# Kernel tuning notes

Hardware: AMD Instinct MI355X
Metric: run time of the kernel (lower is better)

## Reference

```python
import jax, jax.numpy as jnp
import numpy as np

B, M, D, H, C = 256, 512, 768, 8, 768


def setup_inputs() -> dict:
    key = jax.random.key(0)
    ks = jax.random.split(key, 12)
    rn = lambda k, shp, s=1.0: jax.random.normal(k, shp, dtype=jnp.float32) * s
    w = 1.0 / np.sqrt(D)
    return dict(
        controller_state=rn(ks[0], (B, C)),
        write_data=rn(ks[1], (B, D)),
        memory=rn(ks[2], (M, D), 0.1),
        in_proj_w=rn(ks[3], (3 * D, D), w), in_proj_b=jnp.zeros((3 * D,), jnp.float32),
        out_w=rn(ks[4], (D, D), w), out_b=jnp.zeros((D,), jnp.float32),
        read_w=rn(ks[5], (D, C), w), read_b=jnp.zeros((D,), jnp.float32),
        write_w=rn(ks[6], (D, C), w), write_b=jnp.zeros((D,), jnp.float32),
        erase_w=rn(ks[7], (D, C), w), erase_b=jnp.zeros((D,), jnp.float32),
        ug_w=rn(ks[8], (1, C + D), w), ug_b=jnp.zeros((1,), jnp.float32),
        fg_w=rn(ks[9], (1, C + D), w), fg_b=jnp.zeros((1,), jnp.float32),
    )


def _mha(q, kv, in_proj_w, in_proj_b, out_w, out_b, num_heads):
    # q: [B,1,D] query, kv: [B,M,D] keys=values. Matches torch.nn.MultiheadAttention
    # (batch_first, eval mode -> no dropout, average_attn_weights=True).
    b, m, d = kv.shape
    dh = d // num_heads
    wq, wk, wv = jnp.split(in_proj_w, 3, axis=0)
    bq, bk, bv = jnp.split(in_proj_b, 3, axis=0)
    qh = (q @ wq.T + bq).reshape(b, 1, num_heads, dh).transpose(0, 2, 1, 3)   # [B,H,1,dh]
    kh = (kv @ wk.T + bk).reshape(b, m, num_heads, dh).transpose(0, 2, 1, 3)  # [B,H,M,dh]
    vh = (kv @ wv.T + bv).reshape(b, m, num_heads, dh).transpose(0, 2, 1, 3)
    scores = jnp.einsum('bhqd,bhkd->bhqk', qh, kh) / jnp.sqrt(jnp.float32(dh))
    attn = jax.nn.softmax(scores, axis=-1)                                    # [B,H,1,M]
    ctx = jnp.einsum('bhqk,bhkd->bhqd', attn, vh)
    ctx = ctx.transpose(0, 2, 1, 3).reshape(b, 1, d)
    out = ctx @ out_w.T + out_b
    return out, attn.mean(axis=1)  # out [B,1,D], weights averaged over heads [B,1,M]


def reference(controller_state, write_data, memory, in_proj_w, in_proj_b,
              out_w, out_b, read_w, read_b, write_w, write_b,
              erase_w, erase_b, ug_w, ug_b, fg_w, fg_b):
    b = controller_state.shape[0]
    memory_batch = jnp.broadcast_to(memory[None], (b,) + memory.shape)        # [B,M,D]

    read_key = (controller_state @ read_w.T + read_b)[:, None, :]             # [B,1,D]
    read_data, _ = _mha(read_key, memory_batch, in_proj_w, in_proj_b, out_w, out_b, H)
    read_data = read_data[:, 0, :]                                            # [B,D]

    write_key = (controller_state @ write_w.T + write_b)[:, None, :]
    erase_vec = jax.nn.sigmoid(controller_state @ erase_w.T + erase_b)[:, None, :]  # [B,1,D]
    _, write_weights = _mha(write_key, memory_batch, in_proj_w, in_proj_b, out_w, out_b, H)
    ww = write_weights[:, 0, :]                                               # [B,M]

    combined = jnp.concatenate([controller_state, read_data], axis=-1)        # [B,C+D]
    ug = jax.nn.sigmoid(combined @ ug_w.T + ug_b)                             # [B,1]
    fg = jax.nn.sigmoid(combined @ fg_w.T + fg_b)                             # [B,1]

    erase_term = ww[:, :, None] * erase_vec * fg[:, :, None]                  # [B,M,D]
    write_term = ww[:, :, None] * write_data[:, None, :] * ug[:, :, None]     # [B,M,D]
    updated_memory = memory_batch + (write_term - erase_term)
    return read_data, updated_memory
```

## Files before the change

### kernel.cpp

```cpp
#include <hip/hip_runtime.h>
#include <hip/hip_bf16.h>
#include <math.h>

#define B_ 256
#define M_ 512
#define D_ 768
#define H_ 8
#define DH_ 96
#define C_ 768

typedef float  f32x4_t __attribute__((ext_vector_type(4)));
typedef short  s16x8   __attribute__((ext_vector_type(8)));
typedef unsigned short u16;

__device__ __forceinline__ u16 cvt_bf16(float f) {
    __hip_bfloat16 h = __float2bfloat16(f);
    union { __hip_bfloat16 h; u16 u; } v; v.h = h;
    return v.u;
}
__device__ __forceinline__ float bf16_f32(u16 h) {
    union { unsigned int u; float f; } v; v.u = ((unsigned int)h) << 16;
    return v.f;
}

#define ACC_INIT {{0,0,0,0},{0,0,0,0},{0,0,0,0},{0,0,0,0}}
#define SCALE_ 0.10206207261596577f

template<int BK>
__device__ __forceinline__ void mm64b(
    const u16* __restrict__ A, int lda, const u16* __restrict__ B, int ldb,
    int ksteps, int bRowClamp, u16* lA, u16* lB, f32x4_t* acc, int nfrag)
{
    constexpr int NL = BK / 32;
    const int t = threadIdx.x;
    const int srow = t >> 2, kq = t & 3;
    const int l = t & 63, w = t >> 6;
    const int brow = srow < bRowClamp ? srow : bRowClamp;

    s16x8 va[NL], vb[NL];
    #pragma unroll
    for (int c = 0; c < NL; ++c) {
        const int ko = (kq * NL + c) * 8;
        va[c] = *reinterpret_cast<const s16x8*>(A + (size_t)srow * lda + ko);
        vb[c] = *reinterpret_cast<const s16x8*>(B + (size_t)brow * ldb + ko);
    }

    for (int ks = 0; ks < ksteps; ++ks) {
        __syncthreads();
        #pragma unroll
        for (int c = 0; c < NL; ++c) {
            const int kb = kq * NL + c;
            *reinterpret_cast<s16x8*>(lA + (kb * 64 + srow) * 8) = va[c];
            *reinterpret_cast<s16x8*>(lB + (kb * 64 + srow) * 8) = vb[c];
        }
        __syncthreads();
        if (ks + 1 < ksteps) {
            #pragma unroll
            for (int c = 0; c < NL; ++c) {
                const int ko = (ks + 1) * BK + (kq * NL + c) * 8;
                va[c] = *reinterpret_cast<const s16x8*>(A + (size_t)srow * lda + ko);
                vb[c] = *reinterpret_cast<const s16x8*>(B + (size_t)brow * ldb + ko);
            }
        }
        #pragma unroll
        for (int ksub = 0; ksub < NL; ++ksub) {
            const int kb = (l >> 4) + ksub * 4;
            s16x8 af = *reinterpret_cast<const s16x8*>(lA + (kb * 64 + w * 16 + (l & 15)) * 8);
            #pragma unroll
            for (int nb = 0; nb < 4; ++nb) {
                if (nb < nfrag) {
                    s16x8 bf = *reinterpret_cast<const s16x8*>(lB + (kb * 64 + nb * 16 + (l & 15)) * 8);
                    acc[nb] = __builtin_amdgcn_mfma_f32_16x16x32_bf16(af, bf, acc[nb], 0, 0, 0);
                }
            }
        }
    }
}

__device__ __forceinline__ void epilogue_f32(
    const f32x4_t* acc, float* out, int ldo, int m0, int n0,
    const float* bias, int act, int nfrag)
{
    const int t = threadIdx.x, l = t & 63, w = t >> 6;
    const int mbase = m0 + w * 16 + (l >> 4) * 4;
    #pragma unroll
    for (int nb = 0; nb < 4; ++nb) {
        if (nb >= nfrag) break;
        const int col = n0 + nb * 16 + (l & 15);
        const float bv = bias ? bias[col] : 0.0f;
        #pragma unroll
        for (int r = 0; r < 4; ++r) {
            float v = acc[nb][r] + bv;
            if (act) v = 1.0f / (1.0f + expf(-v));
            out[(size_t)(mbase + r) * ldo + col] = v;
        }
    }
}

__device__ __forceinline__ void epilogue_bf16(
    const f32x4_t* acc, u16* out, int ldo, int m0, int n0,
    const float* bias, int nfrag)
{
    const int t = threadIdx.x, l = t & 63, w = t >> 6;
    const int mbase = m0 + w * 16 + (l >> 4) * 4;
    #pragma unroll
    for (int nb = 0; nb < 4; ++nb) {
        if (nb >= nfrag) break;
        const int col = n0 + nb * 16 + (l & 15);
        const float bv = bias ? bias[col] : 0.0f;
        #pragma unroll
        for (int r = 0; r < 4; ++r)
            out[(size_t)(mbase + r) * ldo + col] = cvt_bf16(acc[nb][r] + bv);
    }
}

__global__ __launch_bounds__(256) void conv_kernel(
    const float* __restrict__ mem, const float* __restrict__ cs,
    const float* __restrict__ ipw, const float* __restrict__ rw,
    const float* __restrict__ www, const float* __restrict__ ew,
    const float* __restrict__ outw, const float* __restrict__ outb,
    const float* __restrict__ ugw, const float* __restrict__ ugb,
    const float* __restrict__ fgw, const float* __restrict__ fgb,
    u16* __restrict__ memb, u16* __restrict__ csb, u16* __restrict__ ipwb,
    u16* __restrict__ rwb, u16* __restrict__ wwwb, u16* __restrict__ ewb,
    u16* __restrict__ outwb, float* __restrict__ vg, float* __restrict__ gc)
{
    __shared__ float sred[256];
    const int bid = blockIdx.x, t = threadIdx.x;

    if (bid < 2304) {
        const float* src; u16* dst; int base;
        if      (bid < 192)  { src = mem;  dst = memb;  base = bid; }
        else if (bid < 288)  { src = cs;   dst = csb;   base = bid - 192; }
        else if (bid < 1152) { src = ipw;  dst = ipwb;  base = bid - 288; }
        else if (bid < 1440) { src = rw;   dst = rwb;   base = bid - 1152; }
        else if (bid < 1728) { src = www;  dst = wwwb;  base = bid - 1440; }
        else if (bid < 2016) { src = ew;   dst = ewb;   base = bid - 1728; }
        else                 { src = outw; dst = outwb; base = bid - 2016; }
        const size_t i = ((size_t)base * 256 + t) * 8;
        float4 x = *reinterpret_cast<const float4*>(src + i);
        float4 y = *reinterpret_cast<const float4*>(src + i + 4);
        s16x8 o;
        o[0]=cvt_bf16(x.x); o[1]=cvt_bf16(x.y); o[2]=cvt_bf16(x.z); o[3]=cvt_bf16(x.w);
        o[4]=cvt_bf16(y.x); o[5]=cvt_bf16(y.y); o[6]=cvt_bf16(y.z); o[7]=cvt_bf16(y.w);
        *reinterpret_cast<s16x8*>(dst + i) = o;
    } else {
        const int lid = bid - 2304;
        const int v = lid / 12, kt = lid % 12;
        const float* gw = v == 0 ? ugw : fgw;
        const int c = t & 63, g = t >> 6;
        const int col = kt * 64 + c;
        float acc = 0.f;
        #pragma unroll 4
        for (int i = 0; i < 192; ++i) {
            const int row = g * 192 + i;
            acc += outw[(size_t)row * 768 + col] * gw[768 + row];
        }
        sred[t] = acc;
        __syncthreads();
        if (g == 0)
            vg[v * 768 + col] = sred[c] + sred[64 + c] + sred[128 + c] + sred[192 + c];
        if (kt == 0) {
            __syncthreads();
            float cp = outb[t] * gw[768 + t] + outb[t + 256] * gw[768 + t + 256]
                     + outb[t + 512] * gw[768 + t + 512];
            sred[t] = cp; __syncthreads();
            #pragma unroll
            for (int off = 128; off > 0; off >>= 1) {
                if (t < off) sred[t] += sred[t + off];
                __syncthreads();
            }
            if (t == 0) gc[v] = sred[0] + (v == 0 ? ugb[0] : fgb[0]);
        }
    }
}

__global__ __launch_bounds__(256) void stage1_kernel(
    const u16* __restrict__ memb, const u16* __restrict__ csb,
    const u16* __restrict__ ipwb, const float* __restrict__ ipb,
    const u16* __restrict__ rwb, const float* __restrict__ rb,
    const u16* __restrict__ wwwb, const float* __restrict__ ww_b,
    const u16* __restrict__ ewb, const float* __restrict__ eb,
    u16* __restrict__ khb, u16* __restrict__ vhT,
    u16* __restrict__ rwkeysb, float* __restrict__ erase)
{
    __shared__ u16 lA[8192], lB[8192];
    f32x4_t acc[4] = ACC_INIT;
    const int bid = blockIdx.x;
    if (bid < 192) {
        const int mt = bid / 24, nt = bid % 24;
        mm64b<64>(memb + (size_t)mt * 64 * 768, 768,
                  ipwb + (size_t)768 * 768 + (size_t)nt * 64 * 768, 768,
                  12, 63, lA, lB, acc, 4);
        const int t = threadIdx.x, l = t & 63, w = t >> 6;
        const int mbase = mt * 64 + w * 16 + (l >> 4) * 4;
        if (nt < 12) {
            #pragma unroll
            for (int nb = 0; nb < 4; ++nb) {
                const int col = nt * 64 + nb * 16 + (l & 15);
                const float bv = ipb[768 + col];
                #pragma unroll
                for (int r = 0; r < 4; ++r)
                    khb[(size_t)(mbase + r) * 768 + col] = cvt_bf16(acc[nb][r] + bv);
            }
        } else {
            #pragma unroll
            for (int nb = 0; nb < 4; ++nb) {
                const int cg = (nt - 12) * 64 + nb * 16 + (l & 15);
                const int h = cg / 96, d = cg % 96;
                const float bv = ipb[1536 + cg];
                u16* dst = vhT + ((size_t)h * 96 + d) * 512;
                #pragma unroll
                for (int r = 0; r < 4; ++r)
                    dst[mbase + r] = cvt_bf16(acc[nb][r] + bv);
            }
        }
    } else if (bid < 240) {
        const int lid = bid - 192, mt = lid / 12, nt = lid % 12;
        mm64b<64>(csb + (size_t)mt * 64 * 768, 768, rwb + (size_t)nt * 64 * 768, 768,
                  12, 63, lA, lB, acc, 4);
        epilogue_bf16(acc, rwkeysb, 768, mt * 64, nt * 64, rb, 4);
    } else if (bid < 288) {
        const int lid = bid - 240, mt = lid / 12, nt = lid % 12;
        mm64b<64>(csb + (size_t)mt * 64 * 768, 768, wwwb + (size_t)nt * 64 * 768, 768,
                  12, 63, lA, lB, acc, 4);
        epilogue_bf16(acc, rwkeysb + (size_t)256 * 768, 768, mt * 64, nt * 64, ww_b, 4);
    } else {
        const int lid = bid - 288, mt = lid / 12, nt = lid % 12;
        mm64b<64>(csb + (size_t)mt * 64 * 768, 768, ewb + (size_t)nt * 64 * 768, 768,
                  12, 63, lA, lB, acc, 4);
        epilogue_f32(acc, erase, 768, mt * 64, nt * 64, eb, 1, 4);
    }
}

__global__ __launch_bounds__(256) void stage2_kernel(
    const u16* __restrict__ rwkeysb, const u16* __restrict__ ipwb,
    const float* __restrict__ ipb, u16* __restrict__ qrwb)
{
    __shared__ u16 lA[8192], lB[8192];
    f32x4_t acc[4] = ACC_INIT;
    const int mt = blockIdx.x / 12, nt = blockIdx.x % 12;
    mm64b<64>(rwkeysb + (size_t)mt * 64 * 768, 768, ipwb + (size_t)nt * 64 * 768, 768,
              12, 63, lA, lB, acc, 4);
    epilogue_bf16(acc, qrwb, 768, mt * 64, nt * 64, ipb, 4);
}

__global__ __launch_bounds__(256) void scores_kernel(
    const u16* __restrict__ qrwb, const u16* __restrict__ khb, u16* __restrict__ E)
{
    __shared__ u16 lA[2048], lB[2048];
    f32x4_t acc[4] = ACC_INIT;
    const int h = blockIdx.y;
    const int mt = blockIdx.x >> 3, nt = blockIdx.x & 7;
    mm64b<32>(qrwb + (size_t)mt * 64 * 768 + h * 96, 768,
              khb + (size_t)nt * 64 * 768 + h * 96, 768, 3, 63, lA, lB, acc, 4);
    const int t = threadIdx.x, l = t & 63, w = t >> 6;
    const int mbase = mt * 64 + w * 16 + (l >> 4) * 4;
    #pragma unroll
    for (int nb = 0; nb < 4; ++nb) {
        const int col = nt * 64 + nb * 16 + (l & 15);
        #pragma unroll
        for (int r = 0; r < 4; ++r) {
            const float e = expf(fminf(acc[nb][r] * SCALE_, 30.0f));
            E[((size_t)h * 512 + mbase + r) * 512 + col] = cvt_bf16(e);
        }
    }
}

__global__ __launch_bounds__(256) void pvww_kernel(
    const u16* __restrict__ E, const u16* __restrict__ vhT, u16* __restrict__ ctxb,
    float* __restrict__ wwb)
{
    const int bid = blockIdx.x, t = threadIdx.x;
    if (bid < 64) {
        __shared__ u16 lA[8192], lB[8192];
        __shared__ float rinv[64];
        f32x4_t acc[4] = ACC_INIT;
        const int h = bid >> 3;
        const int mt = (bid >> 1) & 3, nt = bid & 1;
        const int n0 = nt * 64;
        const int nfrag = nt == 0 ? 4 : 2;
        const int bclamp = nt == 0 ? 63 : 31;

        const u16* A  = E + ((size_t)h * 512 + mt * 64) * 512;
        const u16* Bv = vhT + ((size_t)h * 96 + n0) * 512;

        const int srow = t >> 2, kq = t & 3;
        const int l = t & 63, w = t >> 6;
        const int brow = srow < bclamp ? srow : bclamp;

        s16x8 va[2], vb[2];
        #pragma unroll
        for (int c = 0; c < 2; ++c) {
            const int ko = (kq * 2 + c) * 8;
            va[c] = *reinterpret_cast<const s16x8*>(A + (size_t)srow * 512 + ko);
            vb[c] = *reinterpret_cast<const s16x8*>(Bv + (size_t)brow * 512 + ko);
        }

        float rs = 0.f;
        for (int ks = 0; ks < 8; ++ks) {
            __syncthreads();
            #pragma unroll
            for (int c = 0; c < 2; ++c) {
                const int kb = kq * 2 + c;
                *reinterpret_cast<s16x8*>(lA + (kb * 64 + srow) * 8) = va[c];
                *reinterpret_cast<s16x8*>(lB + (kb * 64 + srow) * 8) = vb[c];
            }
            #pragma unroll
            for (int c = 0; c < 2; ++c)
                #pragma unroll
                for (int j = 0; j < 8; ++j)
                    rs += bf16_f32((u16)va[c][j]);
            __syncthreads();
            if (ks + 1 < 8) {
                #pragma unroll
                for (int c = 0; c < 2; ++c) {
                    const int ko = (ks + 1) * 64 + (kq * 2 + c) * 8;
                    va[c] = *reinterpret_cast<const s16x8*>(A + (size_t)srow * 512 + ko);
                    vb[c] = *reinterpret_cast<const s16x8*>(Bv + (size_t)brow * 512 + ko);
                }
            }
            #pragma unroll
            for (int ksub = 0; ksub < 2; ++ksub) {
                const int kb = (l >> 4) + ksub * 4;
                s16x8 af = *reinterpret_cast<const s16x8*>(lA + (kb * 64 + w * 16 + (l & 15)) * 8);
                #pragma unroll
                for (int nb = 0; nb < 4; ++nb) {
                    if (nb < nfrag) {
                        s16x8 bf = *reinterpret_cast<const s16x8*>(lB + (kb * 64 + nb * 16 + (l & 15)) * 8);
                        acc[nb] = __builtin_amdgcn_mfma_f32_16x16x32_bf16(af, bf, acc[nb], 0, 0, 0);
                    }
                }
            }
        }
        rs += __shfl_xor(rs, 1);
        rs += __shfl_xor(rs, 2);
        if (kq == 0) rinv[srow] = 1.0f / rs;
        __syncthreads();

        const int mbase = w * 16 + (l >> 4) * 4;
        #pragma unroll
        for (int nb = 0; nb < 4; ++nb) {
            if (nb >= nfrag) break;
            const int col = n0 + nb * 16 + (l & 15);
            #pragma unroll
            for (int r = 0; r < 4; ++r) {
                const float v = acc[nb][r] * rinv[mbase + r];
                ctxb[(size_t)(mt * 64 + mbase + r) * 768 + h * 96 + col] = cvt_bf16(v);
            }
        }
    } else {
        const int b = bid - 64;
        __shared__ float linv8[8];
        const int w = t >> 6, l = t & 63;
        #pragma unroll
        for (int hh = 0; hh < 2; ++hh) {
            const int h = w * 2 + hh;
            const u16* row = E + ((size_t)h * 512 + 256 + b) * 512;
            float s = 0.f;
            #pragma unroll
            for (int c = 0; c < 8; ++c) s += bf16_f32(row[c * 64 + l]);
            #pragma unroll
            for (int off = 32; off > 0; off >>= 1) s += __shfl_xor(s, off);
            if (l == 0) linv8[h] = 1.0f / s;
        }
        __syncthreads();
        #pragma unroll
        for (int mm_ = 0; mm_ < 2; ++mm_) {
            const int m = t + mm_ * 256;
            float s = 0.f;
            #pragma unroll
            for (int h = 0; h < H_; ++h)
                s += bf16_f32(E[((size_t)h * 512 + 256 + b) * 512 + m]) * linv8[h];
            wwb[(size_t)b * 512 + m] = s * 0.125f;
        }
    }
}

__global__ __launch_bounds__(256) void gates_kernel(
    const u16* __restrict__ ctxb,
    const float* __restrict__ cs,
    const float* __restrict__ ugw, const float* __restrict__ fgw,
    const float* __restrict__ vg, const float* __restrict__ gc,
    float* __restrict__ ugfg)
{
    const int b = blockIdx.x, t = threadIdx.x;
    __shared__ float red[8];
    float pu = 0.f, pf = 0.f;
    #pragma unroll
    for (int c = 0; c < 3; ++c) {
        const int i = t + c * 256;
        const float cv = cs[(size_t)b * 768 + i];
        const float xv = bf16_f32(ctxb[(size_t)b * 768 + i]);
        pu += cv * ugw[i] + xv * vg[i];
        pf += cv * fgw[i] + xv * vg[768 + i];
    }
    const int w = t >> 6, l = t & 63;
    #pragma unroll
    for (int off = 32; off > 0; off >>= 1) {
        pu += __shfl_xor(pu, off);
        pf += __shfl_xor(pf, off);
    }
    if (l == 0) { red[w] = pu; red[4 + w] = pf; }
    __syncthreads();
    if (t == 0) {
        ugfg[2 * b]     = 1.0f / (1.0f + expf(-(red[0] + red[1] + red[2] + red[3] + gc[0])));
        ugfg[2 * b + 1] = 1.0f / (1.0f + expf(-(red[4] + red[5] + red[6] + red[7] + gc[1])));
    }
}

__global__ __launch_bounds__(256) void final_kernel(
    const u16* __restrict__ ctxb, const u16* __restrict__ outwb,
    const float* __restrict__ outb, float* __restrict__ rd_out,
    const float* __restrict__ mem, const float* __restrict__ wwb,
    const float* __restrict__ wdta, const float* __restrict__ erase,
    const float* __restrict__ ugfg, float* __restrict__ mem_out)
{
    __shared__ u16 lA[8192], lB[8192];
    const int bid = blockIdx.x, t = threadIdx.x;
    if (bid < 48) {
        f32x4_t acc[4] = ACC_INIT;
        const int mt = bid / 12, nt = bid % 12;
        mm64b<64>(ctxb + (size_t)mt * 64 * 768, 768, outwb + (size_t)nt * 64 * 768, 768,
                  12, 63, lA, lB, acc, 4);
        epilogue_f32(acc, rd_out, 768, mt * 64, nt * 64, outb, 0, 4);
    } else {
        const int u = bid - 48;
        const int b  = u >> 6;
        const int m0 = (u & 63) << 3;
        const float ug = ugfg[2 * b], fg = ugfg[2 * b + 1];
        const f32x4_t* m4 = reinterpret_cast<const f32x4_t*>(mem);
        f32x4_t* o4 = reinterpret_cast<f32x4_t*>(mem_out + (size_t)b * 393216);
        const float* wrow = wdta  + (size_t)b * 768;
        const float* erow = erase + (size_t)b * 768;
        #pragma unroll
        for (int ph = 0; ph < 6; ++ph) {
            const int c = t + ph * 256;
            const int m = m0 + c / 192;
            const int d4 = c % 192;
            const float w = wwb[(size_t)b * 512 + m];
            const f32x4_t wd = *reinterpret_cast<const f32x4_t*>(wrow + d4 * 4);
            const f32x4_t er = *reinterpret_cast<const f32x4_t*>(erow + d4 * 4);
            const f32x4_t dd = wd * ug - er * fg;
            f32x4_t mm = m4[(size_t)m * 192 + d4];
            f32x4_t r = mm + w * dd;
            __builtin_nontemporal_store(r, &o4[(size_t)m * 192 + d4]);
        }
    }
}

extern "C" void kernel_launch(void* const* d_in, const int* in_sizes, int n_in,
                              void* d_out, int out_size, void* d_ws, size_t ws_size,
                              hipStream_t stream)
{
    const float* cs   = (const float*)d_in[0];
    const float* wdta = (const float*)d_in[1];
    const float* mem  = (const float*)d_in[2];
    const float* ipw  = (const float*)d_in[3];
    const float* ipb  = (const float*)d_in[4];
    const float* outw = (const float*)d_in[5];
    const float* outb = (const float*)d_in[6];
    const float* rw   = (const float*)d_in[7];
    const float* rb   = (const float*)d_in[8];
    const float* ww_w = (const float*)d_in[9];
    const float* ww_b = (const float*)d_in[10];
    const float* ew   = (const float*)d_in[11];
    const float* eb   = (const float*)d_in[12];
    const float* ugw  = (const float*)d_in[13];
    const float* ugb  = (const float*)d_in[14];
    const float* fgw  = (const float*)d_in[15];
    const float* fgb  = (const float*)d_in[16];

    float* rd_out  = (float*)d_out;
    float* mem_out = (float*)d_out + B_ * D_;

    float* S0 = mem_out;
    u16*   memb    = (u16*)(S0 + 0);
    u16*   csb     = (u16*)(S0 + 196608);
    u16*   ipwb    = (u16*)(S0 + 294912);
    u16*   rwb     = (u16*)(S0 + 1179648);
    u16*   wwwb    = (u16*)(S0 + 1474560);
    u16*   ewb     = (u16*)(S0 + 1769472);
    u16*   khb     = (u16*)(S0 + 2064384);
    u16*   vhT     = (u16*)(S0 + 2260992);
    u16*   rwkeysb = (u16*)(S0 + 2457600);
    u16*   qrwb    = (u16*)(S0 + 2654208);

    float* ws    = (float*)d_ws;
    float* erase = ws;
    u16*   ctxb  = (u16*)(ws + 196608);
    u16*   E     = (u16*)(ws + 294912);
    float* vg    =        ws + 1343488;
    float* gc    =        ws + 1345024;
    float* ugfg  =        ws + 1345040;
    float* wwb   =        ws + 1345552;
    u16*   outwb = (u16*)(ws + 1476624);

    conv_kernel<<<2328, 256, 0, stream>>>(mem, cs, ipw, rw, ww_w, ew, outw, outb,
                                          ugw, ugb, fgw, fgb,
                                          memb, csb, ipwb, rwb, wwwb, ewb, outwb,
                                          vg, gc);
    stage1_kernel<<<336, 256, 0, stream>>>(memb, csb, ipwb, ipb, rwb, rb, wwwb, ww_b,
                                           ewb, eb, khb, vhT, rwkeysb, erase);
    stage2_kernel<<<96, 256, 0, stream>>>(rwkeysb, ipwb, ipb, qrwb);
    scores_kernel<<<dim3(64, 8), 256, 0, stream>>>(qrwb, khb, E);
    pvww_kernel<<<320, 256, 0, stream>>>(E, vhT, ctxb, wwb);
    gates_kernel<<<256, 256, 0, stream>>>(ctxb, cs, ugw, fgw, vg, gc, ugfg);
    final_kernel<<<16432, 256, 0, stream>>>(ctxb, outwb, outb, rd_out,
                                            mem, wwb, wdta, erase, ugfg, mem_out);
}
```

Before: 126.6 us.

## Fold gate projection through value matrix to remove gates kernel launch

```diff
diff --git a/kernel.cpp b/kernel.cpp
--- a/kernel.cpp
+++ b/kernel.cpp
@@ -235,14 +235,31 @@
 
 __global__ __launch_bounds__(256) void stage2_kernel(
     const u16* __restrict__ rwkeysb, const u16* __restrict__ ipwb,
-    const float* __restrict__ ipb, u16* __restrict__ qrwb)
-{
-    __shared__ u16 lA[8192], lB[8192];
-    f32x4_t acc[4] = ACC_INIT;
-    const int mt = blockIdx.x / 12, nt = blockIdx.x % 12;
-    mm64b<64>(rwkeysb + (size_t)mt * 64 * 768, 768, ipwb + (size_t)nt * 64 * 768, 768,
-              12, 63, lA, lB, acc, 4);
-    epilogue_bf16(acc, qrwb, 768, mt * 64, nt * 64, ipb, 4);
+    const float* __restrict__ ipb, u16* __restrict__ qrwb,
+    const u16* __restrict__ vhT, const float* __restrict__ vg,
+    float* __restrict__ zv)
+{
+    const int bid = blockIdx.x, t = threadIdx.x;
+    if (bid < 96) {
+        __shared__ u16 lA[8192], lB[8192];
+        f32x4_t acc[4] = ACC_INIT;
+        const int mt = bid / 12, nt = bid % 12;
+        mm64b<64>(rwkeysb + (size_t)mt * 64 * 768, 768, ipwb + (size_t)nt * 64 * 768, 768,
+                  12, 63, lA, lB, acc, 4);
+        epilogue_bf16(acc, qrwb, 768, mt * 64, nt * 64, ipb, 4);
+    } else {
+        const int lid = bid - 96;
+        const int v = lid >> 3, h = lid & 7;
+        float a0 = 0.f, a1 = 0.f;
+        for (int d = 0; d < 96; ++d) {
+            const float g = vg[v * 768 + h * 96 + d];
+            const u16* row = vhT + ((size_t)h * 96 + d) * 512;
+            a0 += bf16_f32(row[t]) * g;
+            a1 += bf16_f32(row[t + 256]) * g;
+        }
+        zv[(size_t)v * 4096 + h * 512 + t]       = a0;
+        zv[(size_t)v * 4096 + h * 512 + t + 256] = a1;
+    }
 }
 
 __global__ __launch_bounds__(256) void scores_kernel(
@@ -269,7 +286,10 @@
 
 __global__ __launch_bounds__(256) void pvww_kernel(
     const u16* __restrict__ E, const u16* __restrict__ vhT, u16* __restrict__ ctxb,
-    float* __restrict__ wwb)
+    float* __restrict__ wwb,
+    const float* __restrict__ cs, const float* __restrict__ ugw,
+    const float* __restrict__ fgw, const float* __restrict__ zv,
+    const float* __restrict__ gc, float* __restrict__ ugfg)
 {
     const int bid = blockIdx.x, t = threadIdx.x;
     if (bid < 64) {
@@ -349,7 +369,7 @@
                 ctxb[(size_t)(mt * 64 + mbase + r) * 768 + h * 96 + col] = cvt_bf16(v);
             }
         }
-    } else {
+    } else if (bid < 320) {
         const int b = bid - 64;
         __shared__ float linv8[8];
         const int w = t >> 6, l = t & 63;
@@ -374,38 +394,64 @@
                 s += bf16_f32(E[((size_t)h * 512 + 256 + b) * 512 + m]) * linv8[h];
             wwb[(size_t)b * 512 + m] = s * 0.125f;
         }
-    }
-}
-
-__global__ __launch_bounds__(256) void gates_kernel(
-    const u16* __restrict__ ctxb,
-    const float* __restrict__ cs,
-    const float* __restrict__ ugw, const float* __restrict__ fgw,
-    const float* __restrict__ vg, const float* __restrict__ gc,
-    float* __restrict__ ugfg)
-{
-    const int b = blockIdx.x, t = threadIdx.x;
-    __shared__ float red[8];
-    float pu = 0.f, pf = 0.f;
-    #pragma unroll
-    for (int c = 0; c < 3; ++c) {
-        const int i = t + c * 256;
-        const float cv = cs[(size_t)b * 768 + i];
-        const float xv = bf16_f32(ctxb[(size_t)b * 768 + i]);
-        pu += cv * ugw[i] + xv * vg[i];
-        pf += cv * fgw[i] + xv * vg[768 + i];
-    }
-    const int w = t >> 6, l = t & 63;
-    #pragma unroll
-    for (int off = 32; off > 0; off >>= 1) {
-        pu += __shfl_xor(pu, off);
-        pf += __shfl_xor(pf, off);
-    }
-    if (l == 0) { red[w] = pu; red[4 + w] = pf; }
-    __syncthreads();
-    if (t == 0) {
-        ugfg[2 * b]     = 1.0f / (1.0f + expf(-(red[0] + red[1] + red[2] + red[3] + gc[0])));
-        ugfg[2 * b + 1] = 1.0f / (1.0f + expf(-(red[4] + red[5] + red[6] + red[7] + gc[1])));
+    } else {
+        const int b = bid - 320;
+        __shared__ float wred[4][3];
+        __shared__ float gacc[2];
+        __shared__ float red[8];
+        const int w = t >> 6, l = t & 63;
+        if (t == 0) { gacc[0] = 0.f; gacc[1] = 0.f; }
+
+        float pu = 0.f, pf = 0.f;
+        #pragma unroll
+        for (int c = 0; c < 3; ++c) {
+            const int i = t + c * 256;
+            const float cv = cs[(size_t)b * 768 + i];
+            pu += cv * ugw[i];
+            pf += cv * fgw[i];
+        }
+
+        for (int h = 0; h < 8; ++h) {
+            float s0 = 0.f, su = 0.f, sf = 0.f;
+            #pragma unroll
+            for (int mm_ = 0; mm_ < 2; ++mm_) {
+                const int m = t + mm_ * 256;
+                const float e = bf16_f32(E[((size_t)h * 512 + b) * 512 + m]);
+                s0 += e;
+                su += e * zv[(size_t)h * 512 + m];
+                sf += e * zv[4096 + (size_t)h * 512 + m];
+            }
+            #pragma unroll
+            for (int off = 32; off > 0; off >>= 1) {
+                s0 += __shfl_xor(s0, off);
+                su += __shfl_xor(su, off);
+                sf += __shfl_xor(sf, off);
+            }
+            if (l == 0) { wred[w][0] = s0; wred[w][1] = su; wred[w][2] = sf; }
+            __syncthreads();
+            if (t == 0) {
+                const float S0 = wred[0][0] + wred[1][0] + wred[2][0] + wred[3][0];
+                const float Su = wred[0][1] + wred[1][1] + wred[2][1] + wred[3][1];
+                const float Sf = wred[0][2] + wred[1][2] + wred[2][2] + wred[3][2];
+                gacc[0] += Su / S0;
+                gacc[1] += Sf / S0;
+            }
+            __syncthreads();
+        }
+
+        #pragma unroll
+        for (int off = 32; off > 0; off >>= 1) {
+            pu += __shfl_xor(pu, off);
+            pf += __shfl_xor(pf, off);
+        }
+        if (l == 0) { red[w] = pu; red[4 + w] = pf; }
+        __syncthreads();
+        if (t == 0) {
+            const float tu = red[0] + red[1] + red[2] + red[3] + gacc[0] + gc[0];
+            const float tf = red[4] + red[5] + red[6] + red[7] + gacc[1] + gc[1];
+            ugfg[2 * b]     = 1.0f / (1.0f + expf(-tu));
+            ugfg[2 * b + 1] = 1.0f / (1.0f + expf(-tf));
+        }
     }
 }
 
@@ -495,6 +541,7 @@
     float* ugfg  =        ws + 1345040;
     float* wwb   =        ws + 1345552;
     u16*   outwb = (u16*)(ws + 1476624);
+    float* zv    =        ws + 1771536;
 
     conv_kernel<<<2328, 256, 0, stream>>>(mem, cs, ipw, rw, ww_w, ew, outw, outb,
                                           ugw, ugb, fgw, fgb,
@@ -502,10 +549,10 @@
                                           vg, gc);
     stage1_kernel<<<336, 256, 0, stream>>>(memb, csb, ipwb, ipb, rwb, rb, wwwb, ww_b,
                                            ewb, eb, khb, vhT, rwkeysb, erase);
-    stage2_kernel<<<96, 256, 0, stream>>>(rwkeysb, ipwb, ipb, qrwb);
+    stage2_kernel<<<112, 256, 0, stream>>>(rwkeysb, ipwb, ipb, qrwb, vhT, vg, zv);
     scores_kernel<<<dim3(64, 8), 256, 0, stream>>>(qrwb, khb, E);
-    pvww_kernel<<<320, 256, 0, stream>>>(E, vhT, ctxb, wwb);
-    gates_kernel<<<256, 256, 0, stream>>>(ctxb, cs, ugw, fgw, vg, gc, ugfg);
+    pvww_kernel<<<576, 256, 0, stream>>>(E, vhT, ctxb, wwb,
+                                         cs, ugw, fgw, zv, gc, ugfg);
     final_kernel<<<16432, 256, 0, stream>>>(ctxb, outwb, outb, rd_out,
                                             mem, wwb, wdta, erase, ugfg, mem_out);
 }
```

New measurement: 125.3 us, median of 2. No clear change (-1.1%).
